# Performance work log

Measured on AMD Instinct MI355X. Metric: run time of the kernel, lower is better.

The kernel has to match this reference:

```python
import jax, jax.numpy as jnp
import numpy as np

# FalconMamba2 SSM decoder layer: RMSNorm -> Mamba2 mixer (in_proj, causal depthwise
# conv + SiLU, chunked SSD scan, gated RMSNorm, out_proj) -> residual add.
H_DIM = 2048      # hidden_size
D_SSM = 4096      # mamba_expand * hidden_size
NH = 64           # num heads
P = 64            # head_dim = D_SSM // NH
G = 1             # n_groups
N = 128           # ssm state size
K = 4             # conv kernel
CS = 256          # chunk size
EPS = 1e-5


def rmsnorm(x, w, eps=EPS):
    v = jnp.mean(jnp.square(x), axis=-1, keepdims=True)
    return x * jax.lax.rsqrt(v + eps) * w


def setup_inputs() -> dict:
    key = jax.random.key(0)
    ks = jax.random.split(key, 8)
    proj_dim = 2 * D_SSM + 2 * G * N + NH   # 8512
    conv_dim = D_SSM + 2 * G * N            # 4352
    s = 0.02
    return {
        "x": jax.random.normal(ks[0], (1, 2048, H_DIM), jnp.float32),
        "rms_w": jnp.ones((H_DIM,), jnp.float32),
        "W_in": jax.random.normal(ks[1], (proj_dim, H_DIM), jnp.float32) * s,
        "conv_w": jax.random.normal(ks[2], (conv_dim, K), jnp.float32) * 0.2,
        "conv_b": jnp.zeros((conv_dim,), jnp.float32),
        "dt_bias": jax.random.uniform(ks[3], (NH,), jnp.float32,
                                      minval=float(np.log(1e-3)), maxval=float(np.log(0.1))),
        "A_log": jnp.log(jax.random.uniform(ks[4], (NH,), jnp.float32, minval=1.0, maxval=16.0)),
        "D": jax.random.normal(ks[5], (NH,), jnp.float32) * 0.1 + 1.0,
        "norm_w": jnp.ones((D_SSM,), jnp.float32),
        "W_out": jax.random.normal(ks[6], (H_DIM, D_SSM), jnp.float32) * s,
    }


def reference(x, rms_w, W_in, conv_w, conv_b, dt_bias, A_log, D, norm_w, W_out):
    Bsz, L, _ = x.shape
    h = rmsnorm(x, rms_w)                                   # input_layernorm
    proj = jnp.einsum('blh,ph->blp', h, W_in)               # in_proj (no bias)
    z, xBC, dt = jnp.split(proj, [D_SSM, 2 * D_SSM + 2 * G * N], axis=-1)

    # causal depthwise conv1d (kernel K) + SiLU
    xp = jnp.pad(xBC, ((0, 0), (K - 1, 0), (0, 0)))
    xc = conv_b + sum(xp[:, k:k + L, :] * conv_w[:, k] for k in range(K))
    xc = jax.nn.silu(xc)
    xs, Bm, Cm = jnp.split(xc, [D_SSM, D_SSM + G * N], axis=-1)

    dt = jax.nn.softplus(dt + dt_bias)                      # [B,L,NH]
    A = -jnp.exp(A_log)                                     # [NH]

    nc = L // CS
    xs = xs.reshape(Bsz, nc, CS, NH, P)
    Bm = Bm.reshape(Bsz, nc, CS, G, N)
    Cm = Cm.reshape(Bsz, nc, CS, G, N)
    dtc = dt.reshape(Bsz, nc, CS, NH)

    dA = dtc * A                                            # [B,c,l,h]
    dAc = jnp.cumsum(dA, axis=2)
    dAh = jnp.moveaxis(dAc, 3, 2)                           # [B,c,h,l]
    dth = jnp.moveaxis(dtc, 3, 2)                           # [B,c,h,l]

    # intra-chunk (diagonal block) output
    seg = dAh[..., :, None] - dAh[..., None, :]             # [B,c,h,l,s]
    tril = jnp.tril(jnp.ones((CS, CS), bool))
    Lmat = jnp.exp(jnp.where(tril, seg, -jnp.inf))
    CB = jnp.einsum('bclgn,bcsgn->bcls', Cm, Bm)            # G=1 shared across heads
    M = CB[:, :, None] * Lmat * dth[..., None, :]           # [B,c,h,l,s]
    Y_diag = jnp.einsum('bchls,bcshp->bclhp', M, xs)

    # per-chunk final states and inter-chunk recurrence
    decay_states = jnp.exp(dAh[..., -1:] - dAh)             # [B,c,h,l]
    states = jnp.einsum('bclgn,bchl,bclhp->bchpn', Bm, decay_states * dth, xs)
    chunk_decay = jnp.exp(dAh[..., -1])                     # [B,c,h]

    def step(carry, inp):
        dec, st = inp
        return carry * dec[..., None, None] + st, carry     # emit state BEFORE chunk

    st_t = jnp.moveaxis(states, 1, 0)                       # [c,B,h,p,n]
    dec_t = jnp.moveaxis(chunk_decay, 1, 0)                 # [c,B,h]
    _, prev_states = jax.lax.scan(step, jnp.zeros_like(st_t[0]), (dec_t, st_t))
    prev_states = jnp.moveaxis(prev_states, 0, 1)           # [B,c,h,p,n]

    Y_off = jnp.einsum('bclgn,bchpn,bchl->bclhp', Cm, prev_states, jnp.exp(dAh))

    y = (Y_diag + Y_off + xs * D[:, None]).reshape(Bsz, L, D_SSM)
    y = rmsnorm(y * jax.nn.silu(z), norm_w)                 # gated RMSNorm
    out = jnp.einsum('bld,hd->blh', y, W_out)               # out_proj
    return x + out                                          # residual
```

## Files before the change

### kernel.cpp

```cpp
#include <hip/hip_runtime.h>
#include <stdint.h>


typedef __bf16 bf16x8 __attribute__((ext_vector_type(8)));
typedef float  f32x4  __attribute__((ext_vector_type(4)));

#define DEVFN __device__ __forceinline__

DEVFN unsigned short f2b(float f) {
  uint32_t u = __builtin_bit_cast(uint32_t, f);
  u += 0x7fffu + ((u >> 16) & 1u);
  return (unsigned short)(u >> 16);
}
DEVFN float b2f(unsigned short u) {
  uint32_t x = (uint32_t)u << 16;
  return __builtin_bit_cast(float, x);
}
DEVFN bf16x8 pack8(const float (&m)[8]) {
  bf16x8 r;
#pragma unroll
  for (int t = 0; t < 8; ++t) r[t] = (__bf16)m[t];
  return r;
}

DEVFN void tile_map(int bid, int nwg, int nm, int nn, int grp, int& mt, int& nt) {
  const int q = nwg >> 3, r = nwg & 7;
  const int xcd = bid & 7, lid = bid >> 3;
  const int wg = (xcd < r ? xcd * (q + 1) : r * (q + 1) + (xcd - r) * q) + lid;
  const int per = grp * nn;
  const int g = wg / per;
  const int rem = wg - g * per;
  const int lim = nm - g * grp;
  const int gm = lim < grp ? lim : grp;
  mt = g * grp + rem % gm;
  nt = rem / gm;
}

__global__ void f32_to_bf16_two(
    const float* __restrict__ s1, unsigned short* __restrict__ d1,
    long src1, long dst1,
    const float* __restrict__ s2, unsigned short* __restrict__ d2,
    long src2, long dst2) {
  long i = ((long)blockIdx.x * 256 + threadIdx.x) * 4;
  const float* s; unsigned short* d; long srcE;
  if (i < dst1) { s = s1; d = d1; srcE = src1; }
  else {
    i -= dst1;
    if (i >= dst2) return;
    s = s2; d = d2; srcE = src2;
  }
  ushort4 o;
  if (i < srcE) {
    float4 v = *reinterpret_cast<const float4*>(s + i);
    o.x = f2b(v.x); o.y = f2b(v.y); o.z = f2b(v.z); o.w = f2b(v.w);
  } else {
    o.x = 0; o.y = 0; o.z = 0; o.w = 0;
  }
  *reinterpret_cast<ushort4*>(d + i) = o;
}

__global__ __launch_bounds__(256) void rmsnorm_in(
    const float* __restrict__ x, const float* __restrict__ w,
    unsigned short* __restrict__ h) {
  const int row = blockIdx.x;
  const int base = threadIdx.x * 8;
  if (row >= 2048) {
    ushort4 z = {0, 0, 0, 0};
    *reinterpret_cast<ushort4*>(h + (size_t)row * 2048 + base)     = z;
    *reinterpret_cast<ushort4*>(h + (size_t)row * 2048 + base + 4) = z;
    return;
  }
  const float* xr = x + (size_t)row * 2048;
  float4 v0 = *reinterpret_cast<const float4*>(xr + base);
  float4 v1 = *reinterpret_cast<const float4*>(xr + base + 4);
  float ss = v0.x*v0.x + v0.y*v0.y + v0.z*v0.z + v0.w*v0.w
           + v1.x*v1.x + v1.y*v1.y + v1.z*v1.z + v1.w*v1.w;
  __shared__ float red[4];
#pragma unroll
  for (int off = 32; off > 0; off >>= 1) ss += __shfl_xor(ss, off);
  if ((threadIdx.x & 63) == 0) red[threadIdx.x >> 6] = ss;
  __syncthreads();
  ss = red[0] + red[1] + red[2] + red[3];
  const float scale = rsqrtf(ss * (1.0f / 2048.0f) + 1e-5f);
  float vals[8] = {v0.x, v0.y, v0.z, v0.w, v1.x, v1.y, v1.z, v1.w};
  unsigned short o[8];
#pragma unroll
  for (int j = 0; j < 8; ++j) o[j] = f2b(vals[j] * scale * w[base + j]);
  ushort4 a, b;
  a.x = o[0]; a.y = o[1]; a.z = o[2]; a.w = o[3];
  b.x = o[4]; b.y = o[5]; b.z = o[6]; b.w = o[7];
  *reinterpret_cast<ushort4*>(h + (size_t)row * 2048 + base)     = a;
  *reinterpret_cast<ushort4*>(h + (size_t)row * 2048 + base + 4) = b;
}

template<int BM, bool RES>
__global__ __launch_bounds__(256, 2) void gemm_pipe(
    const unsigned short* __restrict__ A, const unsigned short* __restrict__ B,
    float* __restrict__ C, const float* __restrict__ res,
    int K, int Mc, int Nc, int ldc, int nm, int nn, int grp) {
  constexpr int MF = BM / 32;
  __shared__ __align__(16) unsigned short As[2][BM * 64];
  __shared__ __align__(16) unsigned short Bs[2][128 * 64];
  int mt, nt;
  tile_map(blockIdx.x, nm * nn, nm, nn, grp, mt, nt);
  const int m0 = mt * BM;
  const int n0 = nt * 128;
  const int tid  = threadIdx.x;
  const int wid  = tid >> 6;
  const int lane = tid & 63;
  const int wm   = (wid >> 1) * (BM / 2);
  const int wn   = (wid & 1) * 64;
  const int lrow = lane & 15;
  const int lkc  = lane >> 4;

  auto stageA = [&](int buf, int k0) {
#pragma unroll
    for (int i = 0; i < MF; ++i) {
      const int ci = tid + i * 256;
      const int r = ci >> 3, cc = ci & 7;
      const int gc = cc ^ (r & 7);
      __builtin_amdgcn_global_load_lds(
          (const __attribute__((address_space(1))) void*)(A + (size_t)(m0 + r) * K + k0 + gc * 8),
          (__attribute__((address_space(3))) void*)(&As[buf][ci * 8]), 16, 0, 0);
    }
  };
  auto stageB = [&](int buf, int k0) {
#pragma unroll
    for (int i = 0; i < 4; ++i) {
      const int ci = tid + i * 256;
      const int r = ci >> 3, cc = ci & 7;
      const int gc = cc ^ (r & 7);
      __builtin_amdgcn_global_load_lds(
          (const __attribute__((address_space(1))) void*)(B + (size_t)(n0 + r) * K + k0 + gc * 8),
          (__attribute__((address_space(3))) void*)(&Bs[buf][ci * 8]), 16, 0, 0);
    }
  };

  f32x4 acc[MF][4] = {};
  const int nsteps = K >> 6;

  stageA(0, 0); stageB(0, 0);
  if (nsteps > 1) { stageA(1, 64); stageB(1, 64); }
  if (nsteps > 1) asm volatile("s_waitcnt vmcnt(%0)" :: "n"(MF + 4) : "memory");
  else            asm volatile("s_waitcnt vmcnt(0)" ::: "memory");
  __builtin_amdgcn_s_barrier();
  __builtin_amdgcn_sched_barrier(0);

  int cur = 0;
  for (int t = 0; t < nsteps; ++t) {
    bf16x8 af[MF][2], bf[4][2];
#pragma unroll
    for (int m = 0; m < MF; ++m)
#pragma unroll
      for (int kk = 0; kk < 2; ++kk) {
        const int row = wm + m * 16 + lrow;
        const int c = kk * 4 + lkc;
        af[m][kk] = *reinterpret_cast<const bf16x8*>(
            &As[cur][row * 64 + ((c ^ (row & 7)) * 8)]);
      }
#pragma unroll
    for (int n = 0; n < 4; ++n)
#pragma unroll
      for (int kk = 0; kk < 2; ++kk) {
        const int row = wn + n * 16 + lrow;
        const int c = kk * 4 + lkc;
        bf[n][kk] = *reinterpret_cast<const bf16x8*>(
            &Bs[cur][row * 64 + ((c ^ (row & 7)) * 8)]);
      }
    asm volatile("s_waitcnt lgkmcnt(0)" ::: "memory");
    __builtin_amdgcn_sched_barrier(0);
    __builtin_amdgcn_s_barrier();
    if (t + 2 < nsteps) { stageA(cur, (t + 2) * 64); stageB(cur, (t + 2) * 64); }
    __builtin_amdgcn_s_setprio(1);
#pragma unroll
    for (int kk = 0; kk < 2; ++kk)
#pragma unroll
      for (int m = 0; m < MF; ++m)
#pragma unroll
        for (int n = 0; n < 4; ++n)
          acc[m][n] = __builtin_amdgcn_mfma_f32_16x16x32_bf16(af[m][kk], bf[n][kk], acc[m][n], 0, 0, 0);
    __builtin_amdgcn_s_setprio(0);
    if (t + 1 < nsteps) {
      if (t + 2 < nsteps) asm volatile("s_waitcnt vmcnt(%0)" :: "n"(MF + 4) : "memory");
      else                asm volatile("s_waitcnt vmcnt(0)" ::: "memory");
      __builtin_amdgcn_sched_barrier(0);
      __builtin_amdgcn_s_barrier();
    }
    cur ^= 1;
  }

#pragma unroll
  for (int m = 0; m < MF; ++m) {
#pragma unroll
    for (int n = 0; n < 4; ++n) {
      const int col = n0 + wn + n * 16 + lrow;
      if (col < Nc) {
#pragma unroll
        for (int v = 0; v < 4; ++v) {
          const int row = m0 + wm + m * 16 + (lane >> 4) * 4 + v;
          if (row < Mc) {
            const size_t idx = (size_t)row * ldc + col;
            float val = acc[m][n][v];
            if (RES) val += res[idx];
            C[idx] = val;
          }
        }
      }
    }
  }
}

__global__ __launch_bounds__(256) void conv_silu_dt(
    const float* __restrict__ proj, const float* __restrict__ conv_w,
    const float* __restrict__ conv_b, const float* __restrict__ dt_bias,
    float* __restrict__ xs, float* __restrict__ BC,
    unsigned short* __restrict__ BTb, unsigned short* __restrict__ Bsb,
    unsigned short* __restrict__ Cbb, float* __restrict__ dtc) {
  const int cch = blockIdx.x * 256 + threadIdx.x;
  const int l0 = blockIdx.y * 16;
  if (cch < 4352) {
    const float4 w = *reinterpret_cast<const float4*>(conv_w + (size_t)cch * 4);
    const float b = conv_b[cch];
    const float* pcol = proj + 4096 + cch;
    float w0, w1, w2;
    w0 = (l0 >= 3) ? pcol[(size_t)(l0 - 3) * 8512] : 0.0f;
    w1 = (l0 >= 2) ? pcol[(size_t)(l0 - 2) * 8512] : 0.0f;
    w2 = (l0 >= 1) ? pcol[(size_t)(l0 - 1) * 8512] : 0.0f;
#pragma unroll
    for (int i = 0; i < 16; ++i) {
      const int l = l0 + i;
      const float cur = pcol[(size_t)l * 8512];
      float acc = b + w0 * w.x + w1 * w.y + w2 * w.z + cur * w.w;
      w0 = w1; w1 = w2; w2 = cur;
      acc = acc / (1.0f + __expf(-acc));
      if (cch < 4096) {
        xs[(size_t)l * 4096 + cch] = acc;
      } else {
        BC[(size_t)l * 256 + (cch - 4096)] = acc;
        if (cch < 4224) {
          const int n = cch - 4096;
          const unsigned short bb = f2b(acc);
          BTb[((size_t)((l >> 8) * 128) + n) * 256 + (l & 255)] = bb;
          Bsb[(size_t)l * 128 + n] = bb;
        } else {
          const int n = cch - 4224;
          Cbb[(size_t)l * 128 + n] = f2b(acc);
        }
      }
    }
  } else if (cch < 4416) {
    const int hh = cch - 4352;
    const float bias = dt_bias[hh];
#pragma unroll
    for (int i = 0; i < 16; ++i) {
      const int l = l0 + i;
      const float v = proj[(size_t)l * 8512 + 8448 + hh] + bias;
      dtc[(size_t)l * 64 + hh] = (v > 20.0f) ? v : log1pf(expf(v));
    }
  }
}

__global__ __launch_bounds__(256) void cb_mfma(
    const unsigned short* __restrict__ Cbb,
    const unsigned short* __restrict__ Bsb,
    float* __restrict__ CB) {
  const int bx = blockIdx.x;
  const int c = bx >> 3;
  const int l0 = (bx & 7) * 32;
  const int tid = threadIdx.x;
  const int wid = tid >> 6;
  const int lane = tid & 63;
  const int wm = (wid >> 1) * 16;
  const int wn = (wid & 1) * 128;
  const int lrow = lane & 15;
  const int lk = (lane >> 4) * 8;
  const size_t arow = (size_t)(c * 256 + l0 + wm + lrow) * 128;
  f32x4 acc[8] = {};
#pragma unroll
  for (int kk = 0; kk < 4; ++kk) {
    bf16x8 av = *reinterpret_cast<const bf16x8*>(Cbb + arow + kk * 32 + lk);
#pragma unroll
    for (int nf = 0; nf < 8; ++nf) {
      bf16x8 bv = *reinterpret_cast<const bf16x8*>(
          Bsb + (size_t)(c * 256 + wn + nf * 16 + lrow) * 128 + kk * 32 + lk);
      acc[nf] = __builtin_amdgcn_mfma_f32_16x16x32_bf16(av, bv, acc[nf], 0, 0, 0);
    }
  }
#pragma unroll
  for (int nf = 0; nf < 8; ++nf) {
    const int s = wn + nf * 16 + lrow;
#pragma unroll
    for (int v = 0; v < 4; ++v) {
      const int l = l0 + wm + (lane >> 4) * 4 + v;
      CB[((size_t)(c * 256) + l) * 256 + s] = acc[nf][v];
    }
  }
}

__global__ __launch_bounds__(512) void ssd_states_scan(
    const float* __restrict__ xs, const unsigned short* __restrict__ BTb,
    const float* __restrict__ dtc, const float* __restrict__ A_log,
    float* __restrict__ dAc, float* __restrict__ cdec,
    float* __restrict__ statesT) {
  const int bx = blockIdx.x;
  const int c = bx >> 6, h = bx & 63;
  __shared__ __align__(16) unsigned short xwT[64 * 264];
  __shared__ float dAL[256], dtL[256];
  const int tid = threadIdx.x;
  const int lane = tid & 63;
  const int w = tid >> 6;

  if (tid < 256) dtL[tid] = dtc[(size_t)(c * 256 + tid) * 64 + h];
  const float Ah = -__expf(A_log[h]);
  __syncthreads();
  if (tid < 256) dAL[tid] = dtL[tid] * Ah;
  __syncthreads();
  for (int off = 1; off < 256; off <<= 1) {
    const float t = (tid < 256 && tid >= off) ? dAL[tid - off] : 0.0f;
    __syncthreads();
    if (tid < 256) dAL[tid] += t;
    __syncthreads();
  }
  if (tid < 256) dAc[(size_t)bx * 256 + tid] = dAL[tid];
  if (tid == 255) cdec[bx] = __expf(dAL[255]);
  if (tid < 256) dtL[tid] = __expf(dAL[255] - dAL[tid]) * dtL[tid];
  __syncthreads();

#pragma unroll
  for (int it = 0; it < 4; ++it) {
    const int gid = it * 512 + tid;
    const int p = gid & 63;
    const int s0 = (gid >> 6) * 8;
    bf16x8 r;
#pragma unroll
    for (int k = 0; k < 8; ++k)
      r[k] = (__bf16)(xs[(size_t)(c * 256 + s0 + k) * 4096 + h * 64 + p] * dtL[s0 + k]);
    *reinterpret_cast<bf16x8*>(&xwT[p * 264 + s0]) = r;
  }
  __syncthreads();

  const int pb = (w & 3) * 16;
  const int nb = (w >> 2) * 64;
  const int kcol = (lane >> 4) * 8;
  f32x4 acc[4] = {};
  for (int k = 0; k < 8; ++k) {
    bf16x8 av = *reinterpret_cast<const bf16x8*>(&xwT[(pb + (lane & 15)) * 264 + k * 32 + kcol]);
#pragma unroll
    for (int nf = 0; nf < 4; ++nf) {
      bf16x8 bv = *reinterpret_cast<const bf16x8*>(
          BTb + ((size_t)(c * 128) + nb + nf * 16 + (lane & 15)) * 256 + k * 32 + kcol);
      acc[nf] = __builtin_amdgcn_mfma_f32_16x16x32_bf16(av, bv, acc[nf], 0, 0, 0);
    }
  }
  const int rb = (lane >> 4) * 4;
#pragma unroll
  for (int nf = 0; nf < 4; ++nf) {
    const int n = nb + nf * 16 + (lane & 15);
#pragma unroll
    for (int v = 0; v < 4; ++v) {
      const int p = pb + rb + v;
      statesT[(size_t)bx * 8192 + p * 128 + n] = acc[nf][v];
    }
  }
}

__global__ void ssd_scan(const float* __restrict__ statesT,
                         unsigned short* __restrict__ prevb,
                         const float* __restrict__ cdec) {
  const int i = blockIdx.x * 256 + threadIdx.x;
  const int h = i >> 13;
  const int r = i & 8191;
  float carry = 0.0f;
#pragma unroll
  for (int c = 0; c < 8; ++c) {
    const size_t idx = ((size_t)(c * 64 + h)) * 8192 + r;
    const float st = statesT[idx];
    prevb[idx] = f2b(carry);
    carry = carry * cdec[c * 64 + h] + st;
  }
}

__global__ __launch_bounds__(512) void ssd_diag_off(
    const float* xs, const float* __restrict__ BC,
    const float* __restrict__ dtc, const float* __restrict__ dAc,
    const float* __restrict__ CB, const unsigned short* __restrict__ prevb,
    const float* __restrict__ Dp, float* y) {
  const int bx = blockIdx.x;
  const int c = bx >> 6, h = bx & 63;
  __shared__ __align__(16) unsigned short xsT[64 * 264];
  __shared__ float dAL[256], dtL[256], vdt[256];
  const int tid = threadIdx.x;
  const int lane = tid & 63;
  const int w = tid >> 6;

  if (tid < 256) {
    dAL[tid] = dAc[(size_t)bx * 256 + tid];
    dtL[tid] = dtc[(size_t)(c * 256 + tid) * 64 + h];
  }
  __syncthreads();
  if (tid < 256) vdt[tid] = __expf(dAL[tid | 31] - dAL[tid]) * dtL[tid];
#pragma unroll
  for (int it = 0; it < 4; ++it) {
    const int gid = it * 512 + tid;
    const int p = gid & 63;
    const int s0 = (gid >> 6) * 8;
    bf16x8 r;
#pragma unroll
    for (int k = 0; k < 8; ++k)
      r[k] = (__bf16)xs[(size_t)(c * 256 + s0 + k) * 4096 + h * 64 + p];
    *reinterpret_cast<bf16x8*>(&xsT[p * 264 + s0]) = r;
  }
  __syncthreads();

  const int l1 = w * 32 + (lane & 15);
  const int l2 = l1 + 16;
  const int kcol = (lane >> 4) * 8;
  const float dA1 = dAL[l1], dA2 = dAL[l2];
  const float* CBr1 = CB + ((size_t)(c * 256) + l1) * 256;
  const float* CBr2 = CB + ((size_t)(c * 256) + l2) * 256;
  f32x4 acc[2][4] = {};

  for (int j = 0; j < w; ++j) {
    const int s0 = j * 32 + kcol;
    float cb1[8], cb2[8];
    *reinterpret_cast<float4*>(&cb1[0]) = *reinterpret_cast<const float4*>(CBr1 + s0);
    *reinterpret_cast<float4*>(&cb1[4]) = *reinterpret_cast<const float4*>(CBr1 + s0 + 4);
    *reinterpret_cast<float4*>(&cb2[0]) = *reinterpret_cast<const float4*>(CBr2 + s0);
    *reinterpret_cast<float4*>(&cb2[4]) = *reinterpret_cast<const float4*>(CBr2 + s0 + 4);
    const float a = dAL[j * 32 + 31];
    const float u1 = __expf(dA1 - a), u2 = __expf(dA2 - a);
    float m1[8], m2[8];
#pragma unroll
    for (int t = 0; t < 8; ++t) {
      const float uv = vdt[s0 + t];
      m1[t] = cb1[t] * (u1 * uv);
      m2[t] = cb2[t] * (u2 * uv);
    }
    bf16x8 a1 = pack8(m1), a2 = pack8(m2);
#pragma unroll
    for (int nf = 0; nf < 4; ++nf) {
      bf16x8 bv = *reinterpret_cast<const bf16x8*>(
          &xsT[(nf * 16 + (lane & 15)) * 264 + j * 32 + kcol]);
      acc[0][nf] = __builtin_amdgcn_mfma_f32_16x16x32_bf16(a1, bv, acc[0][nf], 0, 0, 0);
      acc[1][nf] = __builtin_amdgcn_mfma_f32_16x16x32_bf16(a2, bv, acc[1][nf], 0, 0, 0);
    }
  }
  {
    const int s0 = w * 32 + kcol;
    float cb1[8], cb2[8];
    *reinterpret_cast<float4*>(&cb1[0]) = *reinterpret_cast<const float4*>(CBr1 + s0);
    *reinterpret_cast<float4*>(&cb1[4]) = *reinterpret_cast<const float4*>(CBr1 + s0 + 4);
    *reinterpret_cast<float4*>(&cb2[0]) = *reinterpret_cast<const float4*>(CBr2 + s0);
    *reinterpret_cast<float4*>(&cb2[4]) = *reinterpret_cast<const float4*>(CBr2 + s0 + 4);
    float m1[8], m2[8];
#pragma unroll
    for (int t = 0; t < 8; ++t) {
      const int s = s0 + t;
      const float e1 = __expf(fminf(dA1 - dAL[s], 0.0f)) * dtL[s];
      const float e2 = __expf(fminf(dA2 - dAL[s], 0.0f)) * dtL[s];
      m1[t] = (s <= l1) ? cb1[t] * e1 : 0.0f;
      m2[t] = (s <= l2) ? cb2[t] * e2 : 0.0f;
    }
    bf16x8 a1 = pack8(m1), a2 = pack8(m2);
#pragma unroll
    for (int nf = 0; nf < 4; ++nf) {
      bf16x8 bv = *reinterpret_cast<const bf16x8*>(
          &xsT[(nf * 16 + (lane & 15)) * 264 + w * 32 + kcol]);
      acc[0][nf] = __builtin_amdgcn_mfma_f32_16x16x32_bf16(a1, bv, acc[0][nf], 0, 0, 0);
      acc[1][nf] = __builtin_amdgcn_mfma_f32_16x16x32_bf16(a2, bv, acc[1][nf], 0, 0, 0);
    }
  }
  {
    const float eA1 = __expf(dA1), eA2 = __expf(dA2);
    const float* Cr1 = BC + ((size_t)(c * 256) + l1) * 256 + 128;
    const float* Cr2 = BC + ((size_t)(c * 256) + l2) * 256 + 128;
    const unsigned short* pv = prevb + (size_t)bx * 8192;
#pragma unroll
    for (int q = 0; q < 4; ++q) {
      const int n0 = q * 32 + kcol;
      float c1[8], c2[8];
      *reinterpret_cast<float4*>(&c1[0]) = *reinterpret_cast<const float4*>(Cr1 + n0);
      *reinterpret_cast<float4*>(&c1[4]) = *reinterpret_cast<const float4*>(Cr1 + n0 + 4);
      *reinterpret_cast<float4*>(&c2[0]) = *reinterpret_cast<const float4*>(Cr2 + n0);
      *reinterpret_cast<float4*>(&c2[4]) = *reinterpret_cast<const float4*>(Cr2 + n0 + 4);
      float m1[8], m2[8];
#pragma unroll
      for (int t = 0; t < 8; ++t) { m1[t] = c1[t] * eA1; m2[t] = c2[t] * eA2; }
      bf16x8 a1 = pack8(m1), a2 = pack8(m2);
#pragma unroll
      for (int nf = 0; nf < 4; ++nf) {
        bf16x8 bv = *reinterpret_cast<const bf16x8*>(
            pv + (size_t)(nf * 16 + (lane & 15)) * 128 + n0);
        acc[0][nf] = __builtin_amdgcn_mfma_f32_16x16x32_bf16(a1, bv, acc[0][nf], 0, 0, 0);
        acc[1][nf] = __builtin_amdgcn_mfma_f32_16x16x32_bf16(a2, bv, acc[1][nf], 0, 0, 0);
      }
    }
  }
  const float Dh = Dp[h];
  const int rb = (lane >> 4) * 4;
#pragma unroll
  for (int mf = 0; mf < 2; ++mf) {
#pragma unroll
    for (int nf = 0; nf < 4; ++nf) {
      const int p = nf * 16 + (lane & 15);
#pragma unroll
      for (int v = 0; v < 4; ++v) {
        const int l = w * 32 + mf * 16 + rb + v;
        y[(size_t)(c * 256 + l) * 4096 + h * 64 + p] =
            acc[mf][nf][v] + Dh * b2f(xsT[p * 264 + l]);
      }
    }
  }
}

__global__ __launch_bounds__(256) void gated_rmsnorm(
    const float* __restrict__ y, const float* __restrict__ proj,
    const float* __restrict__ nw, unsigned short* __restrict__ y2) {
  const int row = blockIdx.x;
  const float* yr = y + (size_t)row * 4096;
  const float* zr = proj + (size_t)row * 8512;
  const int base = threadIdx.x * 16;
  float g[16];
  float ss = 0.0f;
#pragma unroll
  for (int j = 0; j < 16; j += 4) {
    const float4 yv = *reinterpret_cast<const float4*>(yr + base + j);
    const float4 zv = *reinterpret_cast<const float4*>(zr + base + j);
    const float a0 = yv.x * (zv.x / (1.0f + expf(-zv.x)));
    const float a1 = yv.y * (zv.y / (1.0f + expf(-zv.y)));
    const float a2 = yv.z * (zv.z / (1.0f + expf(-zv.z)));
    const float a3 = yv.w * (zv.w / (1.0f + expf(-zv.w)));
    g[j] = a0; g[j+1] = a1; g[j+2] = a2; g[j+3] = a3;
    ss += a0*a0 + a1*a1 + a2*a2 + a3*a3;
  }
  __shared__ float red[4];
#pragma unroll
  for (int off = 32; off > 0; off >>= 1) ss += __shfl_xor(ss, off);
  if ((threadIdx.x & 63) == 0) red[threadIdx.x >> 6] = ss;
  __syncthreads();
  ss = red[0] + red[1] + red[2] + red[3];
  const float scale = rsqrtf(ss * (1.0f / 4096.0f) + 1e-5f);
#pragma unroll
  for (int j = 0; j < 16; j += 4) {
    ushort4 o;
    o.x = f2b(g[j]   * scale * nw[base + j]);
    o.y = f2b(g[j+1] * scale * nw[base + j + 1]);
    o.z = f2b(g[j+2] * scale * nw[base + j + 2]);
    o.w = f2b(g[j+3] * scale * nw[base + j + 3]);
    *reinterpret_cast<ushort4*>(y2 + (size_t)row * 4096 + base + j) = o;
  }
}

extern "C" void kernel_launch(void* const* d_in, const int* in_sizes, int n_in,
                              void* d_out, int out_size, void* d_ws, size_t ws_size,
                              hipStream_t stream) {
  const float* x       = (const float*)d_in[0];
  const float* rms_w   = (const float*)d_in[1];
  const float* W_in    = (const float*)d_in[2];
  const float* conv_w  = (const float*)d_in[3];
  const float* conv_b  = (const float*)d_in[4];
  const float* dt_bias = (const float*)d_in[5];
  const float* A_log   = (const float*)d_in[6];
  const float* Dp      = (const float*)d_in[7];
  const float* norm_w  = (const float*)d_in[8];
  const float* W_out   = (const float*)d_in[9];
  float* out = (float*)d_out;

  char* ws = (char*)d_ws;
  size_t off = 0;
  auto alloc = [&](size_t bytes) {
    void* p = ws + off;
    off += (bytes + 255) & ~(size_t)255;
    return p;
  };
  unsigned short* Wb_in  = (unsigned short*)alloc((size_t)8576 * 2048 * 2);
  unsigned short* Wb_out = (unsigned short*)alloc((size_t)2048 * 4096 * 2);
  unsigned short* hbuf   = (unsigned short*)alloc((size_t)2112 * 2048 * 2);
  float* proj   = (float*)alloc((size_t)2048 * 8512 * 4);
  float* xsbuf  = (float*)alloc((size_t)2048 * 4096 * 4);
  float* BCbuf  = (float*)alloc((size_t)2048 * 256 * 4);
  unsigned short* BTb = (unsigned short*)alloc((size_t)8 * 128 * 256 * 2);
  unsigned short* Bsb = (unsigned short*)alloc((size_t)2048 * 128 * 2);
  unsigned short* Cbb = (unsigned short*)alloc((size_t)2048 * 128 * 2);
  float* dtcbuf = (float*)alloc((size_t)2048 * 64 * 4);
  float* dAcbuf = (float*)alloc((size_t)512 * 256 * 4);
  float* cdec   = (float*)alloc((size_t)512 * 4);
  float* CBbuf  = (float*)alloc((size_t)8 * 256 * 256 * 4);
  float* statesT = (float*)alloc((size_t)512 * 64 * 128 * 4);
  unsigned short* y2 = Wb_in;
  unsigned short* prevb = hbuf;

  (void)in_sizes; (void)n_in; (void)out_size; (void)ws_size;

  {
    const long d1 = (long)8576 * 2048, s1 = (long)8512 * 2048;
    const long d2 = (long)2048 * 4096, s2 = d2;
    const long chunks = (d1 + d2) / 4;
    f32_to_bf16_two<<<(int)((chunks + 255) / 256), 256, 0, stream>>>(
        W_in, Wb_in, s1, d1, W_out, Wb_out, s2, d2);
  }

  rmsnorm_in<<<2112, 256, 0, stream>>>(x, rms_w, hbuf);

  gemm_pipe<192, false><<<11 * 67, 256, 0, stream>>>(hbuf, Wb_in, proj, nullptr,
                                                     2048, 2048, 8512, 8512,
                                                     11, 67, 4);

  conv_silu_dt<<<dim3(18, 128), 256, 0, stream>>>(proj, conv_w, conv_b, dt_bias,
                                                  xsbuf, BCbuf, BTb, Bsb, Cbb,
                                                  dtcbuf);

  cb_mfma<<<64, 256, 0, stream>>>(Cbb, Bsb, CBbuf);

  ssd_states_scan<<<512, 512, 0, stream>>>(xsbuf, BTb, dtcbuf, A_log,
                                           dAcbuf, cdec, statesT);

  ssd_scan<<<2048, 256, 0, stream>>>(statesT, prevb, cdec);

  ssd_diag_off<<<512, 512, 0, stream>>>(xsbuf, BCbuf, dtcbuf, dAcbuf, CBbuf,
                                        prevb, Dp, xsbuf);

  gated_rmsnorm<<<2048, 256, 0, stream>>>(xsbuf, proj, norm_w, y2);

  gemm_pipe<64, true><<<32 * 16, 256, 0, stream>>>(y2, Wb_out, out, x,
                                                   4096, 2048, 2048, 2048,
                                                   32, 16, 4);
}
```

Baseline: 276.1 us.

## Store SSM x/y intermediates in bf16 and triple-buffer out_proj GEMM

Changes the xs/y intermediate buffer from fp32 to bf16, which halves the traffic between conv, states, diag/off and gated RMSNorm kernels. The kernels that consumed fp32 and converted to bf16 now convert on read instead, and the conversion is dropped where the bf16 value goes straight to LDS. A new triple-buffered GEMM (gemm_pipe3) using global_load_lds with a prefetch depth of three replaces the out_proj GEMM. Rounding y to bf16 before the gated norm adds some precision loss, and the three-stage LDS footprint may lower occupancy.

```diff
diff --git a/kernel.cpp b/kernel.cpp
--- a/kernel.cpp
+++ b/kernel.cpp
@@ -210,10 +210,129 @@
   }
 }
 
+template<int BM, bool RES>
+__global__ __launch_bounds__(256, 2) void gemm_pipe3(
+    const unsigned short* __restrict__ A, const unsigned short* __restrict__ B,
+    float* __restrict__ C, const float* __restrict__ res,
+    int K, int Mc, int Nc, int ldc, int nm, int nn, int grp) {
+  constexpr int MF = BM / 32;
+  constexpr int LPS = MF + 4;
+  __shared__ __align__(16) unsigned short As[3][BM * 64];
+  __shared__ __align__(16) unsigned short Bs[3][128 * 64];
+  int mt, nt;
+  tile_map(blockIdx.x, nm * nn, nm, nn, grp, mt, nt);
+  const int m0 = mt * BM;
+  const int n0 = nt * 128;
+  const int tid  = threadIdx.x;
+  const int wid  = tid >> 6;
+  const int lane = tid & 63;
+  const int wm   = (wid >> 1) * (BM / 2);
+  const int wn   = (wid & 1) * 64;
+  const int lrow = lane & 15;
+  const int lkc  = lane >> 4;
+
+  auto stage = [&](int buf, int k0) {
+#pragma unroll
+    for (int i = 0; i < MF; ++i) {
+      const int ci = tid + i * 256;
+      const int r = ci >> 3, cc = ci & 7;
+      const int gc = cc ^ (r & 7);
+      __builtin_amdgcn_global_load_lds(
+          (const __attribute__((address_space(1))) void*)(A + (size_t)(m0 + r) * K + k0 + gc * 8),
+          (__attribute__((address_space(3))) void*)(&As[buf][ci * 8]), 16, 0, 0);
+    }
+#pragma unroll
+    for (int i = 0; i < 4; ++i) {
+      const int ci = tid + i * 256;
+      const int r = ci >> 3, cc = ci & 7;
+      const int gc = cc ^ (r & 7);
+      __builtin_amdgcn_global_load_lds(
+          (const __attribute__((address_space(1))) void*)(B + (size_t)(n0 + r) * K + k0 + gc * 8),
+          (__attribute__((address_space(3))) void*)(&Bs[buf][ci * 8]), 16, 0, 0);
+    }
+  };
+
+  f32x4 acc[MF][4] = {};
+  const int nsteps = K >> 6;
+
+  stage(0, 0);
+  if (nsteps > 1) stage(1, 64);
+  if (nsteps > 2) stage(2, 128);
+  if (nsteps > 2)      asm volatile("s_waitcnt vmcnt(%0)" :: "n"(2 * LPS) : "memory");
+  else if (nsteps > 1) asm volatile("s_waitcnt vmcnt(%0)" :: "n"(LPS) : "memory");
+  else                 asm volatile("s_waitcnt vmcnt(0)" ::: "memory");
+  __builtin_amdgcn_s_barrier();
+  __builtin_amdgcn_sched_barrier(0);
+
+  int cur = 0;
+  for (int t = 0; t < nsteps; ++t) {
+    bf16x8 af[MF][2], bf[4][2];
+#pragma unroll
+    for (int m = 0; m < MF; ++m)
+#pragma unroll
+      for (int kk = 0; kk < 2; ++kk) {
+        const int row = wm + m * 16 + lrow;
+        const int c = kk * 4 + lkc;
+        af[m][kk] = *reinterpret_cast<const bf16x8*>(
+            &As[cur][row * 64 + ((c ^ (row & 7)) * 8)]);
+      }
+#pragma unroll
+    for (int n = 0; n < 4; ++n)
+#pragma unroll
+      for (int kk = 0; kk < 2; ++kk) {
+        const int row = wn + n * 16 + lrow;
+        const int c = kk * 4 + lkc;
+        bf[n][kk] = *reinterpret_cast<const bf16x8*>(
+            &Bs[cur][row * 64 + ((c ^ (row & 7)) * 8)]);
+      }
+    asm volatile("s_waitcnt lgkmcnt(0)" ::: "memory");
+    __builtin_amdgcn_sched_barrier(0);
+    __builtin_amdgcn_s_barrier();
+    if (t + 3 < nsteps) stage(cur, (t + 3) * 64);
+    __builtin_amdgcn_s_setprio(1);
+#pragma unroll
+    for (int kk = 0; kk < 2; ++kk)
+#pragma unroll
+      for (int m = 0; m < MF; ++m)
+#pragma unroll
+        for (int n = 0; n < 4; ++n)
+          acc[m][n] = __builtin_amdgcn_mfma_f32_16x16x32_bf16(af[m][kk], bf[n][kk], acc[m][n], 0, 0, 0);
+    __builtin_amdgcn_s_setprio(0);
+    if (t + 1 < nsteps) {
+      if (t + 3 < nsteps)      asm volatile("s_waitcnt vmcnt(%0)" :: "n"(2 * LPS) : "memory");
+      else if (t + 2 < nsteps) asm volatile("s_waitcnt vmcnt(%0)" :: "n"(LPS) : "memory");
+      else                     asm volatile("s_waitcnt vmcnt(0)" ::: "memory");
+      __builtin_amdgcn_sched_barrier(0);
+      __builtin_amdgcn_s_barrier();
+    }
+    cur = (cur == 2) ? 0 : cur + 1;
+  }
+
+#pragma unroll
+  for (int m = 0; m < MF; ++m) {
+#pragma unroll
+    for (int n = 0; n < 4; ++n) {
+      const int col = n0 + wn + n * 16 + lrow;
+      if (col < Nc) {
+#pragma unroll
+        for (int v = 0; v < 4; ++v) {
+          const int row = m0 + wm + m * 16 + (lane >> 4) * 4 + v;
+          if (row < Mc) {
+            const size_t idx = (size_t)row * ldc + col;
+            float val = acc[m][n][v];
+            if (RES) val += res[idx];
+            C[idx] = val;
+          }
+        }
+      }
+    }
+  }
+}
+
 __global__ __launch_bounds__(256) void conv_silu_dt(
     const float* __restrict__ proj, const float* __restrict__ conv_w,
     const float* __restrict__ conv_b, const float* __restrict__ dt_bias,
-    float* __restrict__ xs, float* __restrict__ BC,
+    unsigned short* __restrict__ xs, float* __restrict__ BC,
     unsigned short* __restrict__ BTb, unsigned short* __restrict__ Bsb,
     unsigned short* __restrict__ Cbb, float* __restrict__ dtc) {
   const int cch = blockIdx.x * 256 + threadIdx.x;
@@ -234,7 +353,7 @@
       w0 = w1; w1 = w2; w2 = cur;
       acc = acc / (1.0f + __expf(-acc));
       if (cch < 4096) {
-        xs[(size_t)l * 4096 + cch] = acc;
+        xs[(size_t)l * 4096 + cch] = f2b(acc);
       } else {
         BC[(size_t)l * 256 + (cch - 4096)] = acc;
         if (cch < 4224) {
@@ -298,7 +417,7 @@
 }
 
 __global__ __launch_bounds__(512) void ssd_states_scan(
-    const float* __restrict__ xs, const unsigned short* __restrict__ BTb,
+    const unsigned short* __restrict__ xs, const unsigned short* __restrict__ BTb,
     const float* __restrict__ dtc, const float* __restrict__ A_log,
     float* __restrict__ dAc, float* __restrict__ cdec,
     float* __restrict__ statesT) {
@@ -334,7 +453,7 @@
     bf16x8 r;
 #pragma unroll
     for (int k = 0; k < 8; ++k)
-      r[k] = (__bf16)(xs[(size_t)(c * 256 + s0 + k) * 4096 + h * 64 + p] * dtL[s0 + k]);
+      r[k] = (__bf16)(b2f(xs[(size_t)(c * 256 + s0 + k) * 4096 + h * 64 + p]) * dtL[s0 + k]);
     *reinterpret_cast<bf16x8*>(&xwT[p * 264 + s0]) = r;
   }
   __syncthreads();
@@ -381,10 +500,10 @@
 }
 
 __global__ __launch_bounds__(512) void ssd_diag_off(
-    const float* xs, const float* __restrict__ BC,
+    const unsigned short* xs, const float* __restrict__ BC,
     const float* __restrict__ dtc, const float* __restrict__ dAc,
     const float* __restrict__ CB, const unsigned short* __restrict__ prevb,
-    const float* __restrict__ Dp, float* y) {
+    const float* __restrict__ Dp, unsigned short* y) {
   const int bx = blockIdx.x;
   const int c = bx >> 6, h = bx & 63;
   __shared__ __align__(16) unsigned short xsT[64 * 264];
@@ -404,11 +523,11 @@
     const int gid = it * 512 + tid;
     const int p = gid & 63;
     const int s0 = (gid >> 6) * 8;
-    bf16x8 r;
+    unsigned short r[8];
 #pragma unroll
     for (int k = 0; k < 8; ++k)
-      r[k] = (__bf16)xs[(size_t)(c * 256 + s0 + k) * 4096 + h * 64 + p];
-    *reinterpret_cast<bf16x8*>(&xsT[p * 264 + s0]) = r;
+      r[k] = xs[(size_t)(c * 256 + s0 + k) * 4096 + h * 64 + p];
+    *reinterpret_cast<uint4*>(&xsT[p * 264 + s0]) = *reinterpret_cast<uint4*>(r);
   }
   __syncthreads();
 
@@ -507,29 +626,31 @@
       for (int v = 0; v < 4; ++v) {
         const int l = w * 32 + mf * 16 + rb + v;
         y[(size_t)(c * 256 + l) * 4096 + h * 64 + p] =
-            acc[mf][nf][v] + Dh * b2f(xsT[p * 264 + l]);
+            f2b(acc[mf][nf][v] + Dh * b2f(xsT[p * 264 + l]));
       }
     }
   }
 }
 
 __global__ __launch_bounds__(256) void gated_rmsnorm(
-    const float* __restrict__ y, const float* __restrict__ proj,
+    const unsigned short* __restrict__ y, const float* __restrict__ proj,
     const float* __restrict__ nw, unsigned short* __restrict__ y2) {
   const int row = blockIdx.x;
-  const float* yr = y + (size_t)row * 4096;
+  const unsigned short* yr = y + (size_t)row * 4096;
   const float* zr = proj + (size_t)row * 8512;
   const int base = threadIdx.x * 16;
+  unsigned short yu[16];
+  *reinterpret_cast<uint4*>(&yu[0]) = *reinterpret_cast<const uint4*>(yr + base);
+  *reinterpret_cast<uint4*>(&yu[8]) = *reinterpret_cast<const uint4*>(yr + base + 8);
   float g[16];
   float ss = 0.0f;
 #pragma unroll
   for (int j = 0; j < 16; j += 4) {
-    const float4 yv = *reinterpret_cast<const float4*>(yr + base + j);
     const float4 zv = *reinterpret_cast<const float4*>(zr + base + j);
-    const float a0 = yv.x * (zv.x / (1.0f + expf(-zv.x)));
-    const float a1 = yv.y * (zv.y / (1.0f + expf(-zv.y)));
-    const float a2 = yv.z * (zv.z / (1.0f + expf(-zv.z)));
-    const float a3 = yv.w * (zv.w / (1.0f + expf(-zv.w)));
+    const float a0 = b2f(yu[j])     * (zv.x / (1.0f + expf(-zv.x)));
+    const float a1 = b2f(yu[j + 1]) * (zv.y / (1.0f + expf(-zv.y)));
+    const float a2 = b2f(yu[j + 2]) * (zv.z / (1.0f + expf(-zv.z)));
+    const float a3 = b2f(yu[j + 3]) * (zv.w / (1.0f + expf(-zv.w)));
     g[j] = a0; g[j+1] = a1; g[j+2] = a2; g[j+3] = a3;
     ss += a0*a0 + a1*a1 + a2*a2 + a3*a3;
   }
@@ -577,7 +698,7 @@
   unsigned short* Wb_out = (unsigned short*)alloc((size_t)2048 * 4096 * 2);
   unsigned short* hbuf   = (unsigned short*)alloc((size_t)2112 * 2048 * 2);
   float* proj   = (float*)alloc((size_t)2048 * 8512 * 4);
-  float* xsbuf  = (float*)alloc((size_t)2048 * 4096 * 4);
+  unsigned short* xsbuf = (unsigned short*)alloc((size_t)2048 * 4096 * 2);
   float* BCbuf  = (float*)alloc((size_t)2048 * 256 * 4);
   unsigned short* BTb = (unsigned short*)alloc((size_t)8 * 128 * 256 * 2);
   unsigned short* Bsb = (unsigned short*)alloc((size_t)2048 * 128 * 2);
@@ -622,7 +743,7 @@
 
   gated_rmsnorm<<<2048, 256, 0, stream>>>(xsbuf, proj, norm_w, y2);
 
-  gemm_pipe<64, true><<<32 * 16, 256, 0, stream>>>(y2, Wb_out, out, x,
-                                                   4096, 2048, 2048, 2048,
-                                                   32, 16, 4);
-}
+  gemm_pipe3<64, true><<<32 * 16, 256, 0, stream>>>(y2, Wb_out, out, x,
+                                                    4096, 2048, 2048, 2048,
+                                                    32, 16, 4);
+}
```

After: 267.9 us. -3.0%, faster.
